# Performance work log

Measured on AMD Instinct MI355X. Metric: run time of the kernel, lower is better.

The kernel has to match this reference:

```python
import math
import jax, jax.numpy as jnp
import numpy as np

B, N, W, D, H = 16, 64, 128, 128, 4

def posenc(L, d):
    pos = jnp.arange(L, dtype=jnp.float32)[:, None]
    div = jnp.exp(jnp.arange(0, d, 2, dtype=jnp.float32) * (-math.log(10000.0) / d))
    pe = jnp.zeros((L, d), jnp.float32)
    pe = pe.at[:, 0::2].set(jnp.sin(pos * div))
    pe = pe.at[:, 1::2].set(jnp.cos(pos * div))
    return pe

def ln(x):
    # torch nn.LayerNorm(x.shape[1:]) created fresh each call: normalize over all non-batch dims, no affine
    ax = tuple(range(1, x.ndim))
    m = x.mean(ax, keepdims=True)
    v = ((x - m) ** 2).mean(ax, keepdims=True)
    return (x - m) / jnp.sqrt(v + 1e-5)

def conv1d(x, w, b):
    # x [B,C,L], w [Cout,Cin,K] (torch layout), VALID padding
    y = jax.lax.conv_general_dilated(x, w, (1,), 'VALID', dimension_numbers=('NCH', 'OIH', 'NCH'))
    return y + b[None, :, None]

def convt1d(x, w, b, stride, pad):
    # torch ConvTranspose1d, w [Cin,Cout,K]
    K = w.shape[2]
    w_ = jnp.flip(w, 2).transpose(1, 0, 2)  # [Cout,Cin,K]
    y = jax.lax.conv_general_dilated(x, w_, (1,), [(K - 1 - pad, K - 1 - pad)],
                                     lhs_dilation=(stride,), dimension_numbers=('NCH', 'OIH', 'NCH'))
    return y + b[None, :, None]

def mha(q, k, v, wi, bi, wo, bo):
    # torch nn.MultiheadAttention(batch_first=True), H heads
    d = q.shape[-1]
    qp = q @ wi[:d].T + bi[:d]
    kp = k @ wi[d:2 * d].T + bi[d:2 * d]
    vp = v @ wi[2 * d:].T + bi[2 * d:]
    def heads(t):
        b_, l_, _ = t.shape
        return t.reshape(b_, l_, H, d // H).transpose(0, 2, 1, 3)
    qh, kh, vh = heads(qp), heads(kp), heads(vp)
    s = jnp.einsum('bhqd,bhkd->bhqk', qh, kh) / jnp.sqrt(jnp.asarray(d // H, qh.dtype))
    o = jnp.einsum('bhqk,bhkd->bhqd', jax.nn.softmax(s, -1), vh)
    b_, l_ = q.shape[0], q.shape[1]
    return o.transpose(0, 2, 1, 3).reshape(b_, l_, d) @ wo.T + bo


def setup_inputs():
    key = jax.random.key(0)
    ks = iter(jax.random.split(key, 64))
    def w(shape, s=0.05):
        return jax.random.normal(next(ks), shape, jnp.float32) * s
    inp = {}
    inp['tokens'] = jax.random.randint(next(ks), (B, N, W), 0, 257, jnp.int32)
    inp['emb_table'] = w((257, D), 1.0)
    for nm in ['ce', 'ct', 'cg', 'ces', 'cts']:
        inp['w_' + nm] = w((D, D, 3))
        inp['b_' + nm] = w((D,))
    inp['mha_wi'] = w((3 * D, D)); inp['mha_bi'] = w((3 * D,))
    inp['mha_wo'] = w((D, D)); inp['mha_bo'] = w((D,))
    s = 1.0 / math.sqrt(D)
    inp['tgt1'] = jax.random.uniform(next(ks), (1, D), jnp.float32, -s, s)
    inp['tgt2'] = jax.random.uniform(next(ks), (1, D), jnp.float32, -s, s)
    for nm in ['mu', 'lv', 'di']:
        inp['w_' + nm] = w((D, D)); inp['b_' + nm] = w((D,))
    inp['eps'] = jax.random.normal(next(ks), (B, D), jnp.float32)
    inp['dk_w'] = w((32, 32)); inp['dk_b'] = w((32,))
    inp['dv_w'] = w((32, 32)); inp['dv_b'] = w((32,))
    inp['wt1'] = w((32, 64, 3)); inp['bt1'] = w((64,))
    inp['wt2'] = w((64, 128, 3)); inp['bt2'] = w((128,))
    for nm in ['sq', 'sk', 'sv']:
        inp[nm + '_w'] = w((128, 128)); inp[nm + '_b'] = w((128,))
    inp['wt3'] = w((128, 128, 3)); inp['bt3'] = w((128,))
    return inp


def reference(tokens, emb_table, w_ce, b_ce, w_ct, b_ct, w_cg, b_cg, w_ces, b_ces, w_cts, b_cts,
              mha_wi, mha_bi, mha_wo, mha_bo, tgt1, tgt2,
              w_mu, b_mu, w_lv, b_lv, w_di, b_di, eps,
              dk_w, dk_b, dv_w, dv_b, wt1, bt1, wt2, bt2,
              sq_w, sq_b, sk_w, sk_b, sv_w, sv_b, wt3, bt3):
    emb = emb_table[tokens] + posenc(W, D)                    # [B,N,W,D]
    flat = emb.reshape(B * N, W, D)                           # batch the per-sample torch loop

    def word_branch(wc, bc, act):
        h = act(conv1d(flat.transpose(0, 2, 1), wc, bc)).transpose(0, 2, 1)  # [BN,W-2,D]
        return mha(h, h, h, mha_wi, mha_bi, mha_wo, mha_bo)

    a_e = jax.nn.elu(word_branch(w_ce, b_ce, jax.nn.elu))
    a_t = jnp.tanh(word_branch(w_ct, b_ct, jnp.tanh))
    xw = ln((a_e * a_t).reshape(B, N, W - 2, D)).reshape(B * N, W - 2, D)

    h = jax.nn.elu(conv1d(xw.transpose(0, 2, 1), w_cg, b_cg)).transpose(0, 2, 1)  # [BN,W-4,D]
    q1 = jnp.broadcast_to(tgt1[None], (B * N, 1, D))
    out = mha(q1, h, h, mha_wi, mha_bi, mha_wo, mha_bo)[:, 0, :].reshape(B, N, D)

    se = out + posenc(N, D)                                   # sentence level

    def sent_branch(wc, bc, act):
        hh = act(conv1d(se.transpose(0, 2, 1), wc, bc)).transpose(0, 2, 1)       # [B,N-2,D]
        return mha(hh, hh, hh, mha_wi, mha_bi, mha_wo, mha_bo)

    s_e = jax.nn.elu(sent_branch(w_ces, b_ces, jax.nn.elu))
    s_t = jnp.tanh(sent_branch(w_cts, b_cts, jnp.tanh))
    xs = ln(s_e * s_t)
    q2 = jnp.broadcast_to(tgt2[None], (B, 1, D))
    doc = mha(q2, xs, xs, mha_wi, mha_bi, mha_wo, mha_bo)[:, 0, :]

    mu = doc @ w_mu.T + b_mu
    lv = doc @ w_lv.T + b_lv
    z = mu + eps * jnp.exp(0.5 * lv)

    h = (z @ w_di.T + b_di).reshape(B, 32, -1)                # [B,32,4]
    L = h.shape[2]
    k = jnp.einsum('oi,bil->bol', dk_w, h) + dk_b[None, :, None]
    v = jnp.einsum('oi,bil->bol', dv_w, h) + dv_b[None, :, None]
    kh = k.reshape(B, H, 8, L)
    vh = v.reshape(B, H, 8, L)
    att = jax.nn.softmax(jnp.einsum('bhdl,bhdm->bhlm', kh, vh) / jnp.sqrt(8.0), -1)
    h = jax.nn.elu(jnp.einsum('bhlm,bhdm->bhld', att, vh).reshape(B, 32, L))
    h = jax.nn.elu(ln(convt1d(h, wt1, bt1, 2, 1)))            # [B,64,7]
    h = jax.nn.elu(ln(convt1d(h, wt2, bt2, 2, 1)))            # [B,128,13]
    L2 = h.shape[2]
    qc = jnp.einsum('oi,bil->bol', sq_w, h) + sq_b[None, :, None]
    kc = jnp.einsum('oi,bil->bol', sk_w, h) + sk_b[None, :, None]
    vc = jnp.einsum('oi,bil->bol', sv_w, h) + sv_b[None, :, None]
    qh = qc.reshape(B, H, 32, L2)
    khh = kc.reshape(B, H, 32, L2)
    att = jax.nn.softmax(jnp.einsum('bhdl,bhdm->bhlm', qh, khh) / jnp.sqrt(32.0), -1)
    vr = vc.reshape(B, H, 32, L2).reshape(B, H, L2, 32)       # faithful torch .view reinterpretation
    h = jax.nn.elu(jnp.einsum('bhlm,bhmd->bhld', att, vr).reshape(B, 128, L2))
    recon = jax.nn.sigmoid(ln(convt1d(h, wt3, bt3, 1, 1)))    # [B,128,13]
    return recon, mu, lv
```

## Files before the change

### kernel.cpp

```cpp
#include <hip/hip_runtime.h>
#include <hip/hip_bf16.h>

typedef __hip_bfloat16 bf16;
typedef __attribute__((ext_vector_type(8))) short bf16x8;
typedef __attribute__((ext_vector_type(4))) float f32x4;

__device__ __forceinline__ float b2f(bf16 x){ return __bfloat162float(x); }
__device__ __forceinline__ bf16  f2b(float x){ return __float2bfloat16(x); }
__device__ __forceinline__ unsigned short b2u(bf16 x){ union{bf16 b; unsigned short u;} c; c.b = x; return c.u; }

#define LOG2E 1.4426950408889634f
#define QSC (0.17677669529663687f * LOG2E)

#define GLD16(gp, lp) __builtin_amdgcn_global_load_lds( \
    (const __attribute__((address_space(1))) void*)(gp), \
    (__attribute__((address_space(3))) void*)(lp), 16, 0, 0)

__device__ __forceinline__ float fexp2(float x){
  float r; asm("v_exp_f32 %0, %1" : "=v"(r) : "v"(x)); return r;
}
__device__ __forceinline__ float fast_exp(float x){ return fexp2(x * LOG2E); }
__device__ __forceinline__ float eluf(float x){ return x > 0.f ? x : fast_exp(x) - 1.f; }
__device__ __forceinline__ float fast_tanh(float x){
  float cx = fminf(fmaxf(x, -15.f), 15.f);
  float t = fexp2(cx * (2.f*LOG2E));
  return (t - 1.f) / (t + 1.f);
}

#define PE_C (-0.07195578415606394f)

__device__ __forceinline__ float pe_val(int pos, int d){
  int j2 = d & ~1;
  float ang = (float)pos * expf((float)j2 * PE_C);
  return (d & 1) ? cosf(ang) : sinf(ang);
}

__device__ __forceinline__ void pack_one(const float* __restrict__ W, bf16* __restrict__ out,
                                         int K, int N, int conv, int qscale, int t){
  int j = t & 7, lane = (t >> 3) & 63;
  int rest = t >> 9; int NT = N >> 4;
  int nt = rest % NT; int kb = rest / NT;
  int k = kb*32 + ((lane >> 4) << 3) + j;
  int n = nt*16 + (lane & 15);
  float v = conv ? W[n*384 + (k & 127)*3 + (k >> 7)] : W[(long)n*K + k];
  if (qscale && n < 128) v *= QSC;
  out[t] = f2b(v);
}

__global__ void k_prep(const float* __restrict__ w_ce, const float* __restrict__ w_ct,
                       const float* __restrict__ w_cg, const float* __restrict__ w_ces,
                       const float* __restrict__ w_cts, const float* __restrict__ wi,
                       const float* __restrict__ wo,
                       bf16* P_CE, bf16* P_CT, bf16* P_CG, bf16* P_CES, bf16* P_CTS,
                       bf16* P_WI, bf16* P_WO, float* __restrict__ pet){
  int bid = blockIdx.x;
  if (bid < 1152){
    int grp = bid / 192; int t = (bid % 192)*256 + threadIdx.x;
    const float* W; bf16* out; int K, N, conv, qs = 0;
    if      (grp == 0){ W = w_ce;  out = P_CE;  K=384; N=128; conv=1; }
    else if (grp == 1){ W = w_ct;  out = P_CT;  K=384; N=128; conv=1; }
    else if (grp == 2){ W = w_cg;  out = P_CG;  K=384; N=128; conv=1; }
    else if (grp == 3){ W = w_ces; out = P_CES; K=384; N=128; conv=1; }
    else if (grp == 4){ W = w_cts; out = P_CTS; K=384; N=128; conv=1; }
    else              { W = wi;    out = P_WI;  K=128; N=384; conv=0; qs=1; }
    pack_one(W, out, K, N, conv, qs, t);
  } else if (bid < 1216){
    int t = (bid - 1152)*256 + threadIdx.x;
    pack_one(wo, P_WO, 128, 128, 0, 0, t);
  } else {
    int i = (bid - 1216)*256 + threadIdx.x;
    if (i < 16384) pet[i] = pe_val(i >> 7, i & 127);
  }
}

__global__ void k_qprep(const float* __restrict__ wi, const float* __restrict__ bi,
                        const float* __restrict__ t1, const float* __restrict__ t2,
                        float* __restrict__ rkv){
  int tid = threadIdx.x;
  __shared__ float qps[256];
  {
    int which = tid >> 7, jj = tid & 127;
    const float* t = which ? t2 : t1;
    float a = bi[jj];
    for (int i = 0; i < 128; ++i) a += wi[jj*128 + i] * t[i];
    qps[tid] = a;
  }
  __syncthreads();
  int i = tid & 127, which = tid >> 7;
  for (int h = 0; h < 4; ++h){
    float a = 0.f;
    for (int d = 0; d < 32; ++d) a += qps[which*128 + h*32 + d] * wi[(128 + h*32 + d)*128 + i];
    rkv[which*512 + h*128 + i] = a;
  }
}

__global__ void k_embed8(const int* __restrict__ tok, const float* __restrict__ tab,
                         const float* __restrict__ pet, bf16* __restrict__ out){
  int t = blockIdx.x*256 + threadIdx.x;
  int q = t & 15;
  int flat = t >> 4; int w = flat & 127;
  int tk = tok[flat];
  const float* ta = tab + tk*128 + q*8;
  const float* pe = pet + (w << 7) + q*8;
  bf16 ob[8];
  #pragma unroll
  for (int i = 0; i < 8; ++i) ob[i] = f2b(ta[i] + pe[i]);
  *(f32x4*)(out + (size_t)t*8) = *(f32x4*)ob;
}

__global__ void k_se(const bf16* __restrict__ in, const float* __restrict__ pet, bf16* __restrict__ out){
  int idx = blockIdx.x*256 + threadIdx.x;
  int d = idx & 127; int n = (idx >> 7) & 63;
  out[idx] = f2b(b2f(in[idx]) + pet[(n << 7) + d]);
}

template<bool GLL>
__global__ __launch_bounds__(256)
void k_gemm_mfma(const bf16* __restrict__ A, const bf16* __restrict__ Bp_, const bf16* __restrict__ Bp2,
                 const float* __restrict__ bias_, const float* __restrict__ bias2,
                 bf16* __restrict__ C_, bf16* __restrict__ C2p,
                 const bf16* __restrict__ mul,
                 int M, int K, int a_lout, int a_lind, int lda,
                 int NT, int n0t, int ldc, int act_, int act2,
                 const float* __restrict__ lnst, int lngrp){
  const bf16* Bp = Bp_; const float* bias = bias_; bf16* C = C_; int act = act_;
  if (blockIdx.z){ Bp = Bp2; bias = bias2; C = C2p; act = act2; }

  __shared__ f32x4 AsV[2][512];
  char* As0 = (char*)AsV[0];
  char* As1 = (char*)AsV[1];
  int tid = threadIdx.x;
  int lane = tid & 63, wave = tid >> 6;
  int wm = wave >> 1, wn = wave & 1;
  int m0 = blockIdx.x*128;
  int by = blockIdx.y;

  long offA[2]; bool okA[2]; float lnm[2], lnr[2]; int sbyte[2];
  #pragma unroll
  for (int p = 0; p < 2; ++p){
    int e = tid + p*256;
    int row, kq;
    if (GLL){
      int x = e;
      row = (((x >> 3) << 1) | (((x >> 2) ^ (x >> 4)) & 1)) & 127;
      kq  = ((((x >> 1) ^ (x >> 3)) & 1) << 1) | ((x ^ (x >> 2) ^ (x >> 4)) & 1);
    } else {
      row = e >> 2; kq = e & 3;
    }
    int m = m0 + row;
    okA[p] = (m < M);
    long off = 0;
    if (okA[p]){
      off = (a_lout > 0) ? (long)(m / a_lout)*a_lind + (long)(m % a_lout)*128 + kq*8
                         : (long)m*lda + kq*8;
    }
    offA[p] = off;
    lnm[p] = 0.f; lnr[p] = 1.f;
    if (!GLL && lnst && okA[p]){ int g = (int)(off / (long)lngrp); lnm[p] = lnst[2*g]; lnr[p] = lnst[2*g+1]; }
    sbyte[p] = (row*64 + kq*16) ^ ((row & 7) << 4);
  }

  const bf16* bptr[4];
  size_t bstep = (size_t)NT*512;
  #pragma unroll
  for (int fn = 0; fn < 4; ++fn){
    int ntile = n0t + by*8 + wn*4 + fn;
    bptr[fn] = Bp + ((size_t)ntile*64 + lane)*8;
  }
  int abyte[4];
  #pragma unroll
  for (int fm = 0; fm < 4; ++fm){
    int row = wm*64 + fm*16 + (lane & 15);
    abyte[fm] = (row*64 + ((lane >> 4) << 4)) ^ ((row & 7) << 4);
  }

  f32x4 acc[4][4];
  #pragma unroll
  for (int i = 0; i < 4; ++i)
    #pragma unroll
    for (int j = 0; j < 4; ++j) acc[i][j] = (f32x4){0.f,0.f,0.f,0.f};

  int nk = K >> 5;

  if constexpr (GLL){
    int ldsw = (tid >> 6)*1024;
    #pragma unroll
    for (int p = 0; p < 2; ++p)
      GLD16(A + offA[p], As0 + p*4096 + ldsw);
    __syncthreads();
    for (int kb = 0; kb < nk; ++kb){
      char* cur = (kb & 1) ? As1 : As0;
      char* nxt = (kb & 1) ? As0 : As1;
      bool more = (kb + 1) < nk;
      if (more){
        #pragma unroll
        for (int p = 0; p < 2; ++p)
          GLD16(A + offA[p] + (kb+1)*32, nxt + p*4096 + ldsw);
      }
      bf16x8 bfr[4];
      #pragma unroll
      for (int fn = 0; fn < 4; ++fn) bfr[fn] = *(const bf16x8*)(bptr[fn] + (size_t)kb*bstep);
      bf16x8 afr[4];
      #pragma unroll
      for (int fm = 0; fm < 4; ++fm) afr[fm] = *(const bf16x8*)(cur + abyte[fm]);
      #pragma unroll
      for (int fm = 0; fm < 4; ++fm)
        #pragma unroll
        for (int fn = 0; fn < 4; ++fn)
          acc[fm][fn] = __builtin_amdgcn_mfma_f32_16x16x32_bf16(afr[fm], bfr[fn], acc[fm][fn], 0, 0, 0);
      __syncthreads();
    }
  } else {
    auto loadA = [&](int p, int kb)->float4{
      float4 v = make_float4(0.f,0.f,0.f,0.f);
      if (okA[p]){
        v = *(const float4*)(A + offA[p] + kb*32);
        if (lnst){
          bf16* pp = (bf16*)&v; bf16 oo[8];
          #pragma unroll
          for (int u = 0; u < 8; ++u) oo[u] = f2b((b2f(pp[u]) - lnm[p]) * lnr[p]);
          v = *(float4*)&oo[0];
        }
      }
      return v;
    };
    float4 va0 = loadA(0, 0), va1 = loadA(1, 0);
    *(float4*)(As0 + sbyte[0]) = va0;
    *(float4*)(As0 + sbyte[1]) = va1;
    __syncthreads();
    for (int kb = 0; kb < nk; ++kb){
      char* cur = (kb & 1) ? As1 : As0;
      char* nxt = (kb & 1) ? As0 : As1;
      bool more = (kb + 1) < nk;
      if (more){ va0 = loadA(0, kb+1); va1 = loadA(1, kb+1); }
      bf16x8 bfr[4];
      #pragma unroll
      for (int fn = 0; fn < 4; ++fn) bfr[fn] = *(const bf16x8*)(bptr[fn] + (size_t)kb*bstep);
      bf16x8 afr[4];
      #pragma unroll
      for (int fm = 0; fm < 4; ++fm) afr[fm] = *(const bf16x8*)(cur + abyte[fm]);
      #pragma unroll
      for (int fm = 0; fm < 4; ++fm)
        #pragma unroll
        for (int fn = 0; fn < 4; ++fn)
          acc[fm][fn] = __builtin_amdgcn_mfma_f32_16x16x32_bf16(afr[fm], bfr[fn], acc[fm][fn], 0, 0, 0);
      if (more){
        *(float4*)(nxt + sbyte[0]) = va0;
        *(float4*)(nxt + sbyte[1]) = va1;
      }
      __syncthreads();
    }
  }

  #pragma unroll
  for (int fm = 0; fm < 4; ++fm){
    #pragma unroll
    for (int r = 0; r < 4; ++r){
      int m = m0 + wm*64 + fm*16 + ((lane >> 4) << 2) + r;
      if (m >= M) continue;
      #pragma unroll
      for (int fn = 0; fn < 4; ++fn){
        int n = by*128 + wn*64 + fn*16 + (lane & 15);
        float v = acc[fm][fn][r] + (bias ? bias[n] : 0.f);
        if (act == 1) v = eluf(v);
        else if (act == 2) v = fast_tanh(v);
        if (mul) v *= b2f(mul[(long)m*ldc + n]);
        C[(long)m*ldc + n] = f2b(v);
      }
    }
  }
}

template<int L>
__global__ __launch_bounds__(256)
void k_attn_fused(const bf16* __restrict__ X, const bf16* __restrict__ Pwi,
                  const float* __restrict__ bi, bf16* __restrict__ o){
  constexpr int KB  = (L + 31) / 32;
  constexpr int MT  = KB * 2;
  constexpr int WMT = MT / 4;
  constexpr int NP  = KB * 32;
  constexpr int PRS = NP * 2;

  __shared__ alignas(16) char As[NP*256];
  __shared__ alignas(16) char Qb[NP*64];
  __shared__ alignas(16) char Kb[NP*64];
  __shared__ alignas(16) char Vt[32*PRS];
  char* Pb = As;

  int tid = threadIdx.x;
  int s = blockIdx.x >> 2, h = blockIdx.x & 3;
  const bf16* xb = X + (size_t)s*L*128;

  {
    constexpr int NCH = (NP*16)/256;
    int ldsw = (tid >> 6)*1024;
    #pragma unroll
    for (int p = 0; p < NCH; ++p){
      int x = p*256 + tid;
      int row = x >> 4;
      int c = (x & 15) ^ (row & 7);
      const bf16* gp = (row < L) ? (xb + (size_t)row*128 + c*8) : xb;
      GLD16(gp, As + p*4096 + ldsw);
    }
  }
  __syncthreads();

  int lane = tid & 63, wave = tid >> 6;
  int col = lane & 15;

  __builtin_amdgcn_s_setprio(1);
  #pragma unroll
  for (int mt = 0; mt < WMT; ++mt){
    int mtile = wave*WMT + mt;
    int arow = mtile*16 + col;
    bf16x8 a4[4];
    #pragma unroll
    for (int kb = 0; kb < 4; ++kb)
      a4[kb] = *(const bf16x8*)(As + ((arow*256 + kb*64 + ((lane >> 4) << 4)) ^ ((arow & 7) << 4)));
    #pragma unroll
    for (int which = 0; which < 3; ++which){
      f32x4 av[2];
      #pragma unroll
      for (int nt = 0; nt < 2; ++nt){
        int ntile = which*8 + h*2 + nt;
        float bia = bi[which*128 + h*32 + nt*16 + col];
        if (which == 0) bia *= QSC;
        av[nt] = (f32x4){bia, bia, bia, bia};
        #pragma unroll
        for (int kb = 0; kb < 4; ++kb){
          bf16x8 bfr = *(const bf16x8*)(Pwi + (((size_t)kb*24 + ntile)*64 + lane)*8);
          av[nt] = __builtin_amdgcn_mfma_f32_16x16x32_bf16(a4[kb], bfr, av[nt], 0, 0, 0);
        }
      }
      #pragma unroll
      for (int r = 0; r < 4; ++r){
        int row = mtile*16 + ((lane >> 4) << 2) + r;
        if (which < 2){
          unsigned pk = (unsigned)b2u(f2b(av[0][r])) | ((unsigned)b2u(f2b(av[1][r])) << 16);
          char* dst = which ? Kb : Qb;
          *(unsigned*)(dst + ((row*64 + col*4) ^ ((row & 7) << 4))) = pk;
        } else {
          int pos = (row & 15)*MT + (row >> 4);
          #pragma unroll
          for (int nt = 0; nt < 2; ++nt){
            int d = nt*16 + col;
            *(bf16*)(Vt + ((d*PRS + pos*2) ^ ((d & 7) << 4))) = f2b(av[nt][r]);
          }
        }
      }
    }
  }
  __builtin_amdgcn_s_setprio(0);
  __syncthreads();

  f32x4 acc[WMT][MT];
  #pragma unroll
  for (int mt = 0; mt < WMT; ++mt)
    #pragma unroll
    for (int nt = 0; nt < MT; ++nt) acc[mt][nt] = (f32x4){0.f,0.f,0.f,0.f};

  bf16x8 af[WMT];
  #pragma unroll
  for (int mt = 0; mt < WMT; ++mt){
    int row = (wave*WMT + mt)*16 + col;
    af[mt] = *(const bf16x8*)(Qb + ((row*64 + ((lane >> 4) << 4)) ^ ((row & 7) << 4)));
  }
  __builtin_amdgcn_s_setprio(1);
  #pragma unroll
  for (int nt = 0; nt < MT; ++nt){
    int rk2 = nt*16 + col;
    bf16x8 bfk = *(const bf16x8*)(Kb + ((rk2*64 + ((lane >> 4) << 4)) ^ ((rk2 & 7) << 4)));
    #pragma unroll
    for (int mt = 0; mt < WMT; ++mt)
      acc[mt][nt] = __builtin_amdgcn_mfma_f32_16x16x32_bf16(af[mt], bfk, acc[mt][nt], 0, 0, 0);
  }
  __builtin_amdgcn_s_setprio(0);

  const bool lastMask = col >= (L - (MT-1)*16);
  float pinv[WMT][4];
  #pragma unroll
  for (int mt = 0; mt < WMT; ++mt){
    #pragma unroll
    for (int r = 0; r < 4; ++r){
      float mx = -1e30f;
      #pragma unroll
      for (int nt = 0; nt < MT; ++nt){
        float v = acc[mt][nt][r];
        if (nt == MT-1 && lastMask){ v = -1e30f; acc[mt][nt][r] = v; }
        mx = fmaxf(mx, v);
      }
      mx = fmaxf(mx, __shfl_xor(mx, 1));
      mx = fmaxf(mx, __shfl_xor(mx, 2));
      mx = fmaxf(mx, __shfl_xor(mx, 4));
      mx = fmaxf(mx, __shfl_xor(mx, 8));
      float sum = 0.f;
      bf16 prow[MT];
      #pragma unroll
      for (int nt = 0; nt < MT; ++nt){
        float p = fexp2(acc[mt][nt][r] - mx);
        prow[nt] = f2b(p);
        sum += p;
      }
      sum += __shfl_xor(sum, 1);
      sum += __shfl_xor(sum, 2);
      sum += __shfl_xor(sum, 4);
      sum += __shfl_xor(sum, 8);
      pinv[mt][r] = 1.f / sum;
      int row = (wave*WMT + mt)*16 + ((lane >> 4) << 2) + r;
      char* dst = Pb + ((row*PRS + col*(MT*2)) ^ ((row & 7) << 4));
      if constexpr (MT == 8) *(f32x4*)dst = *(f32x4*)prow;
      else                   *(float2*)dst = *(float2*)prow;
    }
  }

  #pragma unroll
  for (int mt = 0; mt < WMT; ++mt){
    int mtile = wave*WMT + mt;
    f32x4 o0 = (f32x4){0.f,0.f,0.f,0.f}, o1 = (f32x4){0.f,0.f,0.f,0.f};
    __builtin_amdgcn_s_setprio(1);
    #pragma unroll
    for (int kb = 0; kb < KB; ++kb){
      int row = mtile*16 + col;
      bf16x8 pa = *(const bf16x8*)(Pb + ((row*PRS + kb*64 + ((lane >> 4) << 4)) ^ ((row & 7) << 4)));
      int d0 = col;
      bf16x8 v0 = *(const bf16x8*)(Vt + ((d0*PRS + kb*64 + ((lane >> 4) << 4)) ^ ((d0 & 7) << 4)));
      bf16x8 v1 = *(const bf16x8*)(Vt + (((d0+16)*PRS + kb*64 + ((lane >> 4) << 4)) ^ (((d0+16) & 7) << 4)));
      o0 = __builtin_amdgcn_mfma_f32_16x16x32_bf16(pa, v0, o0, 0, 0, 0);
      o1 = __builtin_amdgcn_mfma_f32_16x16x32_bf16(pa, v1, o1, 0, 0, 0);
    }
    __builtin_amdgcn_s_setprio(0);
    #pragma unroll
    for (int r = 0; r < 4; ++r){
      int row = mtile*16 + ((lane >> 4) << 2) + r;
      if (row < L){
        size_t ob = ((size_t)s*L + row)*128 + h*32 + col;
        o[ob]      = f2b(o0[r] * pinv[mt][r]);
        o[ob + 16] = f2b(o1[r] * pinv[mt][r]);
      }
    }
  }
}

template<int L>
__global__ __launch_bounds__(256)
void k_attn_tgt(const bf16* __restrict__ hin, const float* __restrict__ rk,
                const float* __restrict__ wi, const float* __restrict__ bi,
                bf16* __restrict__ outp){
  __shared__ alignas(16) char Hs[L*256];
  __shared__ float RKs[512];
  __shared__ float Ps[512];
  __shared__ float Cs[512];
  int tid = threadIdx.x, lane = tid & 63, wave = tid >> 6;
  int s = blockIdx.x;
  const bf16* hb = hin + (size_t)s*L*128;
  for (int e = tid; e < L*16; e += 256){
    int row = e >> 4, c = e & 15;
    *(float4*)(Hs + row*256 + ((c ^ (row & 7)) << 4)) = *(const float4*)(hb + row*128 + c*8);
  }
  for (int e = tid; e < 512; e += 256) RKs[e] = rk[e];
  __syncthreads();

  int j0 = lane, j1 = lane + 64;
  float v0 = -1e30f, v1 = -1e30f;
  if (j0 < L){
    float a = 0.f;
    #pragma unroll
    for (int c = 0; c < 16; ++c){
      bf16x8 x = *(const bf16x8*)(Hs + j0*256 + ((c ^ (j0 & 7)) << 4));
      #pragma unroll
      for (int u = 0; u < 8; ++u) a += b2f(((bf16*)&x)[u]) * RKs[wave*128 + c*8 + u];
    }
    v0 = a * 0.17677669529663687f;
  }
  if (j1 < L){
    float a = 0.f;
    #pragma unroll
    for (int c = 0; c < 16; ++c){
      bf16x8 x = *(const bf16x8*)(Hs + j1*256 + ((c ^ (j1 & 7)) << 4));
      #pragma unroll
      for (int u = 0; u < 8; ++u) a += b2f(((bf16*)&x)[u]) * RKs[wave*128 + c*8 + u];
    }
    v1 = a * 0.17677669529663687f;
  }
  float mx = fmaxf(v0, v1);
  #pragma unroll
  for (int off = 32; off; off >>= 1) mx = fmaxf(mx, __shfl_xor(mx, off));
  float e0 = (j0 < L) ? fast_exp(v0 - mx) : 0.f;
  float e1 = (j1 < L) ? fast_exp(v1 - mx) : 0.f;
  float sum = e0 + e1;
  #pragma unroll
  for (int off = 32; off; off >>= 1) sum += __shfl_xor(sum, off);
  float inv = 1.f / sum;
  Ps[wave*128 + j0] = e0 * inv;
  Ps[wave*128 + j1] = e1 * inv;

  int i0 = lane*2;
  float c0 = 0.f, c1 = 0.f;
  for (int j = 0; j < L; ++j){
    float p = Ps[wave*128 + j];
    short2 w2 = *(const short2*)(Hs + j*256 + (((i0 >> 3) ^ (j & 7)) << 4) + (i0 & 7)*2);
    c0 += p * b2f(*(bf16*)&w2.x);
    c1 += p * b2f(*(bf16*)&w2.y);
  }
  Cs[wave*128 + i0]     = c0;
  Cs[wave*128 + i0 + 1] = c1;
  __syncthreads();

  if (tid < 128){
    int h2 = tid >> 5;
    float a = bi[256 + tid];
    const float* wr = wi + (size_t)(256 + tid)*128;
    for (int i = 0; i < 128; ++i) a += wr[i] * Cs[h2*128 + i];
    outp[(size_t)s*128 + tid] = f2b(a);
  }
}

__global__ void k_ln_partial(const bf16* __restrict__ x, float* __restrict__ part, int GS, int P){
  int pi = blockIdx.x % P;
  int chunk8 = GS / P / 8;
  size_t base = (size_t)(blockIdx.x / P)*GS + (size_t)pi*(GS/P);
  float s = 0.f, s2 = 0.f;
  for (int i = threadIdx.x; i < chunk8; i += 256){
    f32x4 raw = *(const f32x4*)(x + base + (size_t)i*8);
    const bf16* xb = (const bf16*)&raw;
    #pragma unroll
    for (int j = 0; j < 8; ++j){ float v = b2f(xb[j]); s += v; s2 += v*v; }
  }
  #pragma unroll
  for (int off = 32; off; off >>= 1){ s += __shfl_xor(s, off); s2 += __shfl_xor(s2, off); }
  __shared__ float sh[8];
  int lane = threadIdx.x & 63, wv = threadIdx.x >> 6;
  if (lane == 0){ sh[wv] = s; sh[4 + wv] = s2; }
  __syncthreads();
  if (threadIdx.x == 0){
    part[blockIdx.x*2]     = sh[0]+sh[1]+sh[2]+sh[3];
    part[blockIdx.x*2 + 1] = sh[4]+sh[5]+sh[6]+sh[7];
  }
}

__global__ void k_ln_fin(const float* __restrict__ part, float* __restrict__ stats, int P, int GS){
  int g = blockIdx.x;
  float s = 0.f, s2 = 0.f;
  for (int i = threadIdx.x; i < P; i += 256){ s += part[(g*P + i)*2]; s2 += part[(g*P + i)*2 + 1]; }
  #pragma unroll
  for (int off = 32; off; off >>= 1){ s += __shfl_xor(s, off); s2 += __shfl_xor(s2, off); }
  __shared__ float sh[8];
  int lane = threadIdx.x & 63, wv = threadIdx.x >> 6;
  if (lane == 0){ sh[wv] = s; sh[4 + wv] = s2; }
  __syncthreads();
  if (threadIdx.x == 0){
    float S = sh[0]+sh[1]+sh[2]+sh[3], S2 = sh[4]+sh[5]+sh[6]+sh[7];
    float mean = S / GS;
    float var = S2 / GS - mean*mean;
    stats[g*2] = mean; stats[g*2 + 1] = rsqrtf(var + 1e-5f);
  }
}

__global__ void k_ln_small_bf16(const bf16* __restrict__ x, bf16* __restrict__ y, int n){
  int g = blockIdx.x;
  const bf16* xb = x + (size_t)g*n;
  bf16* yb = y + (size_t)g*n;
  float s = 0.f, s2 = 0.f;
  for (int i = threadIdx.x; i < n; i += 256){ float v = b2f(xb[i]); s += v; s2 += v*v; }
  #pragma unroll
  for (int off = 32; off; off >>= 1){ s += __shfl_xor(s, off); s2 += __shfl_xor(s2, off); }
  __shared__ float sh[8];  __shared__ float ms[2];
  int lane = threadIdx.x & 63, wv = threadIdx.x >> 6;
  if (lane == 0){ sh[wv] = s; sh[4 + wv] = s2; }
  __syncthreads();
  if (threadIdx.x == 0){
    float S = sh[0]+sh[1]+sh[2]+sh[3], S2 = sh[4]+sh[5]+sh[6]+sh[7];
    float mean = S / n;
    ms[0] = mean; ms[1] = rsqrtf(S2 / n - mean*mean + 1e-5f);
  }
  __syncthreads();
  float mean = ms[0], inv = ms[1];
  for (int i = threadIdx.x; i < n; i += 256) yb[i] = f2b((b2f(xb[i]) - mean)*inv);
}

__global__ void k_ln_small_f32(const float* __restrict__ x, float* __restrict__ y, int n, int act){
  int g = blockIdx.x;
  const float* xb = x + (size_t)g*n;
  float* yb = y + (size_t)g*n;
  float s = 0.f, s2 = 0.f;
  for (int i = threadIdx.x; i < n; i += 256){ float v = xb[i]; s += v; s2 += v*v; }
  #pragma unroll
  for (int off = 32; off; off >>= 1){ s += __shfl_xor(s, off); s2 += __shfl_xor(s2, off); }
  __shared__ float sh[8];  __shared__ float ms[2];
  int lane = threadIdx.x & 63, wv = threadIdx.x >> 6;
  if (lane == 0){ sh[wv] = s; sh[4 + wv] = s2; }
  __syncthreads();
  if (threadIdx.x == 0){
    float S = sh[0]+sh[1]+sh[2]+sh[3], S2 = sh[4]+sh[5]+sh[6]+sh[7];
    float mean = S / n;
    ms[0] = mean; ms[1] = rsqrtf(S2 / n - mean*mean + 1e-5f);
  }
  __syncthreads();
  float mean = ms[0], inv = ms[1];
  for (int i = threadIdx.x; i < n; i += 256){
    float v = (xb[i] - mean)*inv;
    if (act == 1) v = eluf(v);
    else if (act == 3) v = 1.f/(1.f + fast_exp(-v));
    yb[i] = v;
  }
}

__global__ __launch_bounds__(256)
void k_dec_a(const bf16* __restrict__ DOC,
             const float* __restrict__ w_mu, const float* __restrict__ b_mu,
             const float* __restrict__ w_lv, const float* __restrict__ b_lv,
             const float* __restrict__ eps,
             const float* __restrict__ w_di, const float* __restrict__ b_di,
             const float* __restrict__ dk_w, const float* __restrict__ dk_b,
             const float* __restrict__ dv_w, const float* __restrict__ dv_b,
             const float* __restrict__ wt1, const float* __restrict__ bt1,
             float* __restrict__ dout, float* __restrict__ DEC2){
  int b = blockIdx.x, tid = threadIdx.x;
  __shared__ float Zs[128], H3[128], KD[128], VD[128], D1[128];
  __shared__ float C1[448];
  __shared__ float sc[64];
  __shared__ float red[8], ms[2];

  if (tid < 128){
    const bf16* dr = DOC + b*128;
    float mu = b_mu[tid], lv = b_lv[tid];
    for (int i = 0; i < 128; ++i){
      float x = b2f(dr[i]);
      mu += x * w_mu[tid*128 + i];
      lv += x * w_lv[tid*128 + i];
    }
    dout[26624 + b*128 + tid] = mu;
    dout[28672 + b*128 + tid] = lv;
    Zs[tid] = mu + eps[b*128 + tid] * fast_exp(0.5f*lv);
  }
  __syncthreads();
  if (tid < 128){
    float a = b_di[tid];
    for (int i = 0; i < 128; ++i) a += Zs[i] * w_di[tid*128 + i];
    H3[tid] = a;
  }
  __syncthreads();
  if (tid < 128){
    int l = tid & 3, o2 = tid >> 2;
    float ak = dk_b[o2], av = dv_b[o2];
    for (int i = 0; i < 32; ++i){
      float xv = H3[i*4 + l];
      ak += dk_w[o2*32 + i]*xv;
      av += dv_w[o2*32 + i]*xv;
    }
    KD[tid] = ak; VD[tid] = av;
  }
  __syncthreads();
  if (tid < 64){
    int h = tid >> 4, l = (tid >> 2) & 3, m = tid & 3;
    float a = 0.f;
    #pragma unroll
    for (int d = 0; d < 8; ++d) a += KD[(h*8+d)*4 + l] * VD[(h*8+d)*4 + m];
    sc[tid] = a * 0.35355339059327373f;
  }
  __syncthreads();
  if (tid < 16){
    int base = tid*4;
    float mx = fmaxf(fmaxf(sc[base],sc[base+1]),fmaxf(sc[base+2],sc[base+3]));
    float e0=fast_exp(sc[base]-mx), e1=fast_exp(sc[base+1]-mx), e2=fast_exp(sc[base+2]-mx), e3=fast_exp(sc[base+3]-mx);
    float inv = 1.f/(e0+e1+e2+e3);
    sc[base]=e0*inv; sc[base+1]=e1*inv; sc[base+2]=e2*inv; sc[base+3]=e3*inv;
  }
  __syncthreads();
  if (tid < 128){
    int h = tid >> 5, rem = tid & 31, l = rem >> 3, d = rem & 7;
    float a = 0.f;
    #pragma unroll
    for (int m = 0; m < 4; ++m) a += sc[h*16 + l*4 + m] * VD[(h*8+d)*4 + m];
    D1[tid] = eluf(a);
  }
  __syncthreads();
  for (int idx = tid; idx < 448; idx += 256){
    int co = idx / 7, lo = idx % 7;
    float a = bt1[co];
    for (int k = 0; k < 3; ++k){
      int t = lo + 1 - k;
      if (t < 0 || (t & 1)) continue;
      int li = t >> 1; if (li >= 4) continue;
      float aa = 0.f;
      for (int ci = 0; ci < 32; ++ci) aa += D1[ci*4 + li] * wt1[ci*192 + co*3 + k];
      a += aa;
    }
    C1[idx] = a;
  }
  __syncthreads();
  {
    float s = 0.f, s2 = 0.f;
    for (int i = tid; i < 448; i += 256){ float v = C1[i]; s += v; s2 += v*v; }
    #pragma unroll
    for (int o = 32; o; o >>= 1){ s += __shfl_xor(s, o); s2 += __shfl_xor(s2, o); }
    int lane = tid & 63, wv = tid >> 6;
    if (lane == 0){ red[wv] = s; red[4+wv] = s2; }
    __syncthreads();
    if (tid == 0){
      float S = red[0]+red[1]+red[2]+red[3], S2 = red[4]+red[5]+red[6]+red[7];
      float mean = S/448.f; ms[0] = mean; ms[1] = rsqrtf(S2/448.f - mean*mean + 1e-5f);
    }
    __syncthreads();
    float mean = ms[0], inv = ms[1];
    for (int i = tid; i < 448; i += 256)
      DEC2[b*448 + i] = eluf((C1[i]-mean)*inv);
  }
}

__global__ void k_chanproj3(const float* __restrict__ x,
                            const float* __restrict__ w1, const float* __restrict__ b1,
                            const float* __restrict__ w2, const float* __restrict__ b2,
                            const float* __restrict__ w3, const float* __restrict__ b3,
                            float* __restrict__ y1, float* __restrict__ y2, float* __restrict__ y3,
                            int Bn, int C, int L){
  int idx = blockIdx.x*256 + threadIdx.x;
  if (idx >= Bn*C*L) return;
  int l = idx % L; int t2 = idx / L; int o = t2 % C; int b = t2 / C;
  float a1 = b1[o], a2 = b2[o], a3 = b3[o];
  const float* xb = x + (size_t)b*C*L + l;
  for (int i = 0; i < C; ++i){
    float xv = xb[i*L];
    a1 += w1[(size_t)o*C + i]*xv;
    a2 += w2[(size_t)o*C + i]*xv;
    a3 += w3[(size_t)o*C + i]*xv;
  }
  y1[idx] = a1; y2[idx] = a2; y3[idx] = a3;
}

__global__ __launch_bounds__(256)
void k_dec_attn2(const float* __restrict__ qc, const float* __restrict__ kc,
                 const float* __restrict__ vc, float* __restrict__ out){
  int b = blockIdx.x >> 2, h = blockIdx.x & 3, tid = threadIdx.x;
  __shared__ float sc[169];
  const float* qb = qc + b*1664 + h*416;
  const float* kb = kc + b*1664 + h*416;
  const float* vb = vc + b*1664 + h*416;
  if (tid < 169){
    int l = tid/13, m = tid - l*13;
    float a = 0.f;
    #pragma unroll
    for (int d = 0; d < 32; ++d) a += qb[d*13 + l] * kb[d*13 + m];
    sc[tid] = a * 0.17677669529663687f;
  }
  __syncthreads();
  if (tid < 13){
    float mx = -1e30f;
    for (int m = 0; m < 13; ++m) mx = fmaxf(mx, sc[tid*13 + m]);
    float s = 0.f;
    for (int m = 0; m < 13; ++m){ float p = fast_exp(sc[tid*13 + m] - mx); sc[tid*13 + m] = p; s += p; }
    float inv = 1.f/s;
    for (int m = 0; m < 13; ++m) sc[tid*13 + m] *= inv;
  }
  __syncthreads();
  for (int idx = tid; idx < 416; idx += 256){
    int l = idx >> 5, d = idx & 31;
    float a = 0.f;
    for (int m = 0; m < 13; ++m) a += sc[l*13 + m] * vb[m*32 + d];
    out[b*1664 + h*416 + idx] = eluf(a);
  }
}

__global__ __launch_bounds__(256)
void k_convt(const float* __restrict__ x, const float* __restrict__ w,
             const float* __restrict__ bias, float* __restrict__ y,
             int Bn, int Ci, int Co, int Lin, int Lout, int stride, int pad, int nch){
  __shared__ float xs[1664];
  int b = blockIdx.x / nch;
  int c0 = (blockIdx.x % nch)*16;
  int tid = threadIdx.x;
  for (int i = tid; i < Ci*Lin; i += 256) xs[i] = x[(size_t)b*Ci*Lin + i];
  __syncthreads();
  int co = c0 + (tid & 15);
  int lo = tid >> 4;
  if (co >= Co || lo >= Lout) return;
  float a = bias[co];
  for (int k = 0; k < 3; ++k){
    int t = lo + pad - k;
    if (t < 0 || (t % stride)) continue;
    int li = t / stride;
    if (li >= Lin) continue;
    float aa = 0.f;
    for (int ci = 0; ci < Ci; ++ci) aa += xs[ci*Lin + li] * w[(size_t)ci*Co*3 + co*3 + k];
    a += aa;
  }
  y[(size_t)b*Co*Lout + co*Lout + lo] = a;
}

extern "C" void kernel_launch(void* const* d_in, const int* in_sizes, int n_in,
                              void* d_out, int out_size, void* d_ws, size_t ws_size,
                              hipStream_t stream){
  const int*   tokens = (const int*)  d_in[0];
  const float* tab    = (const float*)d_in[1];
  const float* w_ce = (const float*)d_in[2];  const float* b_ce = (const float*)d_in[3];
  const float* w_ct = (const float*)d_in[4];  const float* b_ct = (const float*)d_in[5];
  const float* w_cg = (const float*)d_in[6];  const float* b_cg = (const float*)d_in[7];
  const float* w_ces= (const float*)d_in[8];  const float* b_ces= (const float*)d_in[9];
  const float* w_cts= (const float*)d_in[10]; const float* b_cts= (const float*)d_in[11];
  const float* wi   = (const float*)d_in[12]; const float* bi   = (const float*)d_in[13];
  const float* wo   = (const float*)d_in[14]; const float* bo   = (const float*)d_in[15];
  const float* tgt1 = (const float*)d_in[16]; const float* tgt2 = (const float*)d_in[17];
  const float* w_mu = (const float*)d_in[18]; const float* b_mu = (const float*)d_in[19];
  const float* w_lv = (const float*)d_in[20]; const float* b_lv = (const float*)d_in[21];
  const float* w_di = (const float*)d_in[22]; const float* b_di = (const float*)d_in[23];
  const float* epsb = (const float*)d_in[24];
  const float* dk_w = (const float*)d_in[25]; const float* dk_b = (const float*)d_in[26];
  const float* dv_w = (const float*)d_in[27]; const float* dv_b = (const float*)d_in[28];
  const float* wt1  = (const float*)d_in[29]; const float* bt1  = (const float*)d_in[30];
  const float* wt2  = (const float*)d_in[31]; const float* bt2  = (const float*)d_in[32];
  const float* sq_w = (const float*)d_in[33]; const float* sq_b = (const float*)d_in[34];
  const float* sk_w = (const float*)d_in[35]; const float* sk_b = (const float*)d_in[36];
  const float* sv_w = (const float*)d_in[37]; const float* sv_b = (const float*)d_in[38];
  const float* wt3  = (const float*)d_in[39]; const float* bt3  = (const float*)d_in[40];

  float* dout = (float*)d_out;

  char* ws = (char*)d_ws;
  size_t off = 0;
  auto take = [&](size_t bytes)->char*{ char* p = ws + off; off += (bytes + 255) & ~(size_t)255; return p; };
  bf16* EMB  = (bf16*)take(16777216ull*2);
  bf16* HB   = (bf16*)take(16515072ull*2);
  bf16* OB   = (bf16*)take(16515072ull*2);
  bf16* AE   = (bf16*)take(16515072ull*2);
  bf16* O1   = (bf16*)take(131072ull*2);
  bf16* OUTB = (bf16*)take(131072ull*2);
  bf16* SEB  = (bf16*)take(131072ull*2);
  bf16* SH   = (bf16*)take(126976ull*2);
  bf16* SCT  = (bf16*)take(126976ull*2);
  bf16* SO   = (bf16*)take(126976ull*2);
  bf16* SAE  = (bf16*)take(126976ull*2);
  bf16* XS   = (bf16*)take(126976ull*2);
  bf16* DO1  = (bf16*)take(2048ull*2);
  bf16* DOC  = (bf16*)take(2048ull*2);
  float* RK  = (float*)take(1024*4);
  float* PART= (float*)take(2016ull*2*4);
  float* STATS=(float*)take(32*4);
  float* DEC2= (float*)take(7168*4);
  float* C2  = (float*)take(26624*4);
  float* DEC3= (float*)take(26624*4);
  float* QC  = (float*)take(26624*4);
  float* KC  = (float*)take(26624*4);
  float* VC  = (float*)take(26624*4);
  float* DEC4= (float*)take(26624*4);
  float* C3  = (float*)take(26624*4);
  float* PET = (float*)take(16384*4);
  bf16* P_CE = (bf16*)take(49152ull*2);
  bf16* P_CT = (bf16*)take(49152ull*2);
  bf16* P_CG = (bf16*)take(49152ull*2);
  bf16* P_CES= (bf16*)take(49152ull*2);
  bf16* P_CTS= (bf16*)take(49152ull*2);
  bf16* P_WI = (bf16*)take(49152ull*2);
  bf16* P_WO = (bf16*)take(16384ull*2);
  (void)ws_size; (void)in_sizes; (void)n_in; (void)out_size;

  auto cdiv = [](long a, long b){ return (int)((a + b - 1)/b); };
  auto gemm = [&](const bf16* A, const bf16* Bpp, const float* bias, bf16* C, const bf16* mul,
                  int M, int N, int K, int a_lout, int a_lind, int lda, int NT, int n0t, int ldc, int act,
                  const float* lnst, int lngrp){
    dim3 g(cdiv(M,128), N/128, 1);
    if (lnst)
      k_gemm_mfma<false><<<g, 256, 0, stream>>>(A, Bpp, Bpp, bias, bias, C, C, mul,
                                                M, K, a_lout, a_lind, lda, NT, n0t, ldc, act, act, lnst, lngrp);
    else
      k_gemm_mfma<true><<<g, 256, 0, stream>>>(A, Bpp, Bpp, bias, bias, C, C, mul,
                                               M, K, a_lout, a_lind, lda, NT, n0t, ldc, act, act, nullptr, 0);
  };
  auto gemmz = [&](const bf16* A, const bf16* Bp1, const float* b1, bf16* C1, int act1,
                   const bf16* Bp2, const float* b2, bf16* C2p, int act2,
                   int M, int N, int K, int a_lout, int a_lind, int lda, int NT, int n0t, int ldc){
    dim3 g(cdiv(M,128), N/128, 2);
    k_gemm_mfma<true><<<g, 256, 0, stream>>>(A, Bp1, Bp2, b1, b2, C1, C2p, nullptr,
                                             M, K, a_lout, a_lind, lda, NT, n0t, ldc, act1, act2, nullptr, 0);
  };

  k_prep<<<1280, 256, 0, stream>>>(w_ce, w_ct, w_cg, w_ces, w_cts, wi, wo,
                                   P_CE, P_CT, P_CG, P_CES, P_CTS, P_WI, P_WO, PET);
  k_qprep<<<1, 256, 0, stream>>>(wi, bi, tgt1, tgt2, RK);
  k_embed8<<<8192, 256, 0, stream>>>(tokens, tab, PET, EMB);

  gemmz(EMB, P_CE, b_ce, HB, 1, P_CT, b_ct, OB, 2, 129024, 128, 384, 126, 16384, 0, 8, 0, 128);

  k_attn_fused<126><<<4096, 256, 0, stream>>>(HB, P_WI, bi, EMB);
  gemm(EMB, P_WO, bo, AE, nullptr, 129024, 128, 128, 0, 0, 128, 8, 0, 128, 1, nullptr, 0);

  k_attn_fused<126><<<4096, 256, 0, stream>>>(OB, P_WI, bi, EMB);
  gemm(EMB, P_WO, bo, HB, AE, 129024, 128, 128, 0, 0, 128, 8, 0, 128, 2, nullptr, 0);

  k_ln_partial<<<2016, 256, 0, stream>>>(HB, PART, 1032192, 126);
  k_ln_fin<<<16, 256, 0, stream>>>(PART, STATS, 126, 1032192);

  gemm(HB, P_CG, b_cg, OB, nullptr, 126976, 128, 384, 124, 16128, 0, 8, 0, 128, 1, STATS, 1032192);

  k_attn_tgt<124><<<1024, 256, 0, stream>>>(OB, RK, wi, bi, O1);
  gemm(O1, P_WO, bo, OUTB, nullptr, 1024, 128, 128, 0, 0, 128, 8, 0, 128, 0, nullptr, 0);

  k_se<<<512, 256, 0, stream>>>(OUTB, PET, SEB);

  gemmz(SEB, P_CES, b_ces, SH, 1, P_CTS, b_cts, SCT, 2, 992, 128, 384, 62, 8192, 0, 8, 0, 128);

  k_attn_fused<62><<<64, 256, 0, stream>>>(SH, P_WI, bi, SO);
  gemm(SO, P_WO, bo, SAE, nullptr, 992, 128, 128, 0, 0, 128, 8, 0, 128, 1, nullptr, 0);

  k_attn_fused<62><<<64, 256, 0, stream>>>(SCT, P_WI, bi, SO);
  gemm(SO, P_WO, bo, SH, SAE, 992, 128, 128, 0, 0, 128, 8, 0, 128, 2, nullptr, 0);

  k_ln_small_bf16<<<16, 256, 0, stream>>>(SH, XS, 7936);

  k_attn_tgt<62><<<16, 256, 0, stream>>>(XS, RK + 512, wi, bi, DO1);
  gemm(DO1, P_WO, bo, DOC, nullptr, 16, 128, 128, 0, 0, 128, 8, 0, 128, 0, nullptr, 0);

  k_dec_a<<<16, 256, 0, stream>>>(DOC, w_mu, b_mu, w_lv, b_lv, epsb, w_di, b_di,
                                  dk_w, dk_b, dv_w, dv_b, wt1, bt1, dout, DEC2);
  k_convt<<<16*8, 256, 0, stream>>>(DEC2, wt2, bt2, C2, 16, 64, 128, 7, 13, 2, 1, 8);
  k_ln_small_f32<<<16, 256, 0, stream>>>(C2, DEC3, 1664, 1);
  k_chanproj3<<<cdiv(26624,256), 256, 0, stream>>>(DEC3, sq_w, sq_b, sk_w, sk_b, sv_w, sv_b,
                                                   QC, KC, VC, 16, 128, 13);
  k_dec_attn2<<<64, 256, 0, stream>>>(QC, KC, VC, DEC4);
  k_convt<<<16*8, 256, 0, stream>>>(DEC4, wt3, bt3, C3, 16, 128, 128, 13, 13, 1, 1, 8);
  k_ln_small_f32<<<16, 256, 0, stream>>>(C3, dout, 1664, 3);
}
```

Baseline: 629.5 us.

## Fuse embedding gather, positional add, and LayerNorm partial sums into GEMM kernels

Removes the standalone embedding kernel: the first conv GEMM now gathers token embeddings and adds positional encodings inside its A-tile load, using the non-LDS-direct path. Removes the separate positional-add kernel by adding the positional term in the output-projection GEMM epilogue. Removes the LayerNorm partial-sum pass by accumulating per-block sums and sums of squares in the preceding GEMM epilogue, with 63 partials per group instead of 126. This saves large intermediate writes and reads, but the first GEMM loses its global-to-LDS direct loads and does scattered fp32 table reads.

```diff
diff --git a/kernel.cpp b/kernel.cpp
--- a/kernel.cpp
+++ b/kernel.cpp
@@ -94,26 +94,6 @@
   }
 }
 
-__global__ void k_embed8(const int* __restrict__ tok, const float* __restrict__ tab,
-                         const float* __restrict__ pet, bf16* __restrict__ out){
-  int t = blockIdx.x*256 + threadIdx.x;
-  int q = t & 15;
-  int flat = t >> 4; int w = flat & 127;
-  int tk = tok[flat];
-  const float* ta = tab + tk*128 + q*8;
-  const float* pe = pet + (w << 7) + q*8;
-  bf16 ob[8];
-  #pragma unroll
-  for (int i = 0; i < 8; ++i) ob[i] = f2b(ta[i] + pe[i]);
-  *(f32x4*)(out + (size_t)t*8) = *(f32x4*)ob;
-}
-
-__global__ void k_se(const bf16* __restrict__ in, const float* __restrict__ pet, bf16* __restrict__ out){
-  int idx = blockIdx.x*256 + threadIdx.x;
-  int d = idx & 127; int n = (idx >> 7) & 63;
-  out[idx] = f2b(b2f(in[idx]) + pet[(n << 7) + d]);
-}
-
 template<bool GLL>
 __global__ __launch_bounds__(256)
 void k_gemm_mfma(const bf16* __restrict__ A, const bf16* __restrict__ Bp_, const bf16* __restrict__ Bp2,
@@ -122,11 +102,15 @@
                  const bf16* __restrict__ mul,
                  int M, int K, int a_lout, int a_lind, int lda,
                  int NT, int n0t, int ldc, int act_, int act2,
-                 const float* __restrict__ lnst, int lngrp){
+                 const float* __restrict__ lnst, int lngrp,
+                 const int* __restrict__ tok, const float* __restrict__ tabp,
+                 const float* __restrict__ petp, const float* __restrict__ sepe,
+                 float* __restrict__ part){
   const bf16* Bp = Bp_; const float* bias = bias_; bf16* C = C_; int act = act_;
   if (blockIdx.z){ Bp = Bp2; bias = bias2; C = C2p; act = act2; }
 
   __shared__ f32x4 AsV[2][512];
+  __shared__ float redp[16];
   char* As0 = (char*)AsV[0];
   char* As1 = (char*)AsV[1];
   int tid = threadIdx.x;
@@ -214,12 +198,25 @@
     auto loadA = [&](int p, int kb)->float4{
       float4 v = make_float4(0.f,0.f,0.f,0.f);
       if (okA[p]){
-        v = *(const float4*)(A + offA[p] + kb*32);
-        if (lnst){
-          bf16* pp = (bf16*)&v; bf16 oo[8];
+        long e = offA[p] + kb*32;
+        if (tok){
+          int seq = (int)(e >> 14); int rest = (int)e & 16383;
+          int wrow = rest >> 7, d0 = rest & 127;
+          int t = tok[(seq << 7) + wrow];
+          const float* ta = tabp + t*128 + d0;
+          const float* pe = petp + (wrow << 7) + d0;
+          bf16 oo[8];
           #pragma unroll
-          for (int u = 0; u < 8; ++u) oo[u] = f2b((b2f(pp[u]) - lnm[p]) * lnr[p]);
+          for (int u = 0; u < 8; ++u) oo[u] = f2b(ta[u] + pe[u]);
           v = *(float4*)&oo[0];
+        } else {
+          v = *(const float4*)(A + e);
+          if (lnst){
+            bf16* pp = (bf16*)&v; bf16 oo[8];
+            #pragma unroll
+            for (int u = 0; u < 8; ++u) oo[u] = f2b((b2f(pp[u]) - lnm[p]) * lnr[p]);
+            v = *(float4*)&oo[0];
+          }
         }
       }
       return v;
@@ -252,6 +249,7 @@
     }
   }
 
+  float ps = 0.f, ps2 = 0.f;
   #pragma unroll
   for (int fm = 0; fm < 4; ++fm){
     #pragma unroll
@@ -265,8 +263,20 @@
         if (act == 1) v = eluf(v);
         else if (act == 2) v = fast_tanh(v);
         if (mul) v *= b2f(mul[(long)m*ldc + n]);
+        if (sepe) v += sepe[(m & 63)*128 + n];
+        if (part){ ps += v; ps2 += v*v; }
         C[(long)m*ldc + n] = f2b(v);
       }
+    }
+  }
+  if (part){
+    #pragma unroll
+    for (int o = 32; o; o >>= 1){ ps += __shfl_xor(ps, o); ps2 += __shfl_xor(ps2, o); }
+    if (lane == 0){ redp[wave] = ps; redp[8 + wave] = ps2; }
+    __syncthreads();
+    if (tid == 0){
+      part[blockIdx.x*2]     = redp[0]+redp[1]+redp[2]+redp[3];
+      part[blockIdx.x*2 + 1] = redp[8]+redp[9]+redp[10]+redp[11];
     }
   }
 }
@@ -512,29 +522,6 @@
     const float* wr = wi + (size_t)(256 + tid)*128;
     for (int i = 0; i < 128; ++i) a += wr[i] * Cs[h2*128 + i];
     outp[(size_t)s*128 + tid] = f2b(a);
-  }
-}
-
-__global__ void k_ln_partial(const bf16* __restrict__ x, float* __restrict__ part, int GS, int P){
-  int pi = blockIdx.x % P;
-  int chunk8 = GS / P / 8;
-  size_t base = (size_t)(blockIdx.x / P)*GS + (size_t)pi*(GS/P);
-  float s = 0.f, s2 = 0.f;
-  for (int i = threadIdx.x; i < chunk8; i += 256){
-    f32x4 raw = *(const f32x4*)(x + base + (size_t)i*8);
-    const bf16* xb = (const bf16*)&raw;
-    #pragma unroll
-    for (int j = 0; j < 8; ++j){ float v = b2f(xb[j]); s += v; s2 += v*v; }
-  }
-  #pragma unroll
-  for (int off = 32; off; off >>= 1){ s += __shfl_xor(s, off); s2 += __shfl_xor(s2, off); }
-  __shared__ float sh[8];
-  int lane = threadIdx.x & 63, wv = threadIdx.x >> 6;
-  if (lane == 0){ sh[wv] = s; sh[4 + wv] = s2; }
-  __syncthreads();
-  if (threadIdx.x == 0){
-    part[blockIdx.x*2]     = sh[0]+sh[1]+sh[2]+sh[3];
-    part[blockIdx.x*2 + 1] = sh[4]+sh[5]+sh[6]+sh[7];
   }
 }
 
@@ -823,7 +810,6 @@
   bf16* OB   = (bf16*)take(16515072ull*2);
   bf16* AE   = (bf16*)take(16515072ull*2);
   bf16* O1   = (bf16*)take(131072ull*2);
-  bf16* OUTB = (bf16*)take(131072ull*2);
   bf16* SEB  = (bf16*)take(131072ull*2);
   bf16* SH   = (bf16*)take(126976ull*2);
   bf16* SCT  = (bf16*)take(126976ull*2);
@@ -833,7 +819,7 @@
   bf16* DO1  = (bf16*)take(2048ull*2);
   bf16* DOC  = (bf16*)take(2048ull*2);
   float* RK  = (float*)take(1024*4);
-  float* PART= (float*)take(2016ull*2*4);
+  float* PART= (float*)take(1008ull*2*4);
   float* STATS=(float*)take(32*4);
   float* DEC2= (float*)take(7168*4);
   float* C2  = (float*)take(26624*4);
@@ -856,58 +842,65 @@
   auto cdiv = [](long a, long b){ return (int)((a + b - 1)/b); };
   auto gemm = [&](const bf16* A, const bf16* Bpp, const float* bias, bf16* C, const bf16* mul,
                   int M, int N, int K, int a_lout, int a_lind, int lda, int NT, int n0t, int ldc, int act,
-                  const float* lnst, int lngrp){
+                  const float* lnst, int lngrp, const float* sepe, float* part){
     dim3 g(cdiv(M,128), N/128, 1);
     if (lnst)
       k_gemm_mfma<false><<<g, 256, 0, stream>>>(A, Bpp, Bpp, bias, bias, C, C, mul,
-                                                M, K, a_lout, a_lind, lda, NT, n0t, ldc, act, act, lnst, lngrp);
+                                                M, K, a_lout, a_lind, lda, NT, n0t, ldc, act, act, lnst, lngrp,
+                                                nullptr, nullptr, nullptr, sepe, part);
     else
       k_gemm_mfma<true><<<g, 256, 0, stream>>>(A, Bpp, Bpp, bias, bias, C, C, mul,
-                                               M, K, a_lout, a_lind, lda, NT, n0t, ldc, act, act, nullptr, 0);
+                                               M, K, a_lout, a_lind, lda, NT, n0t, ldc, act, act, nullptr, 0,
+                                               nullptr, nullptr, nullptr, sepe, part);
+  };
+  auto gemmz_emb = [&](const bf16* Bp1, const float* b1, bf16* C1, int act1,
+                       const bf16* Bp2, const float* b2, bf16* C2p, int act2,
+                       int M, int N, int K, int a_lout, int a_lind, int NT, int ldc){
+    dim3 g(cdiv(M,128), N/128, 2);
+    k_gemm_mfma<false><<<g, 256, 0, stream>>>(nullptr, Bp1, Bp2, b1, b2, C1, C2p, nullptr,
+                                              M, K, a_lout, a_lind, 0, NT, 0, ldc, act1, act2, nullptr, 0,
+                                              tokens, tab, PET, nullptr, nullptr);
   };
   auto gemmz = [&](const bf16* A, const bf16* Bp1, const float* b1, bf16* C1, int act1,
                    const bf16* Bp2, const float* b2, bf16* C2p, int act2,
                    int M, int N, int K, int a_lout, int a_lind, int lda, int NT, int n0t, int ldc){
     dim3 g(cdiv(M,128), N/128, 2);
     k_gemm_mfma<true><<<g, 256, 0, stream>>>(A, Bp1, Bp2, b1, b2, C1, C2p, nullptr,
-                                             M, K, a_lout, a_lind, lda, NT, n0t, ldc, act1, act2, nullptr, 0);
+                                             M, K, a_lout, a_lind, lda, NT, n0t, ldc, act1, act2, nullptr, 0,
+                                             nullptr, nullptr, nullptr, nullptr, nullptr);
   };
 
   k_prep<<<1280, 256, 0, stream>>>(w_ce, w_ct, w_cg, w_ces, w_cts, wi, wo,
                                    P_CE, P_CT, P_CG, P_CES, P_CTS, P_WI, P_WO, PET);
   k_qprep<<<1, 256, 0, stream>>>(wi, bi, tgt1, tgt2, RK);
-  k_embed8<<<8192, 256, 0, stream>>>(tokens, tab, PET, EMB);
-
-  gemmz(EMB, P_CE, b_ce, HB, 1, P_CT, b_ct, OB, 2, 129024, 128, 384, 126, 16384, 0, 8, 0, 128);
+
+  gemmz_emb(P_CE, b_ce, HB, 1, P_CT, b_ct, OB, 2, 129024, 128, 384, 126, 16384, 8, 128);
 
   k_attn_fused<126><<<4096, 256, 0, stream>>>(HB, P_WI, bi, EMB);
-  gemm(EMB, P_WO, bo, AE, nullptr, 129024, 128, 128, 0, 0, 128, 8, 0, 128, 1, nullptr, 0);
+  gemm(EMB, P_WO, bo, AE, nullptr, 129024, 128, 128, 0, 0, 128, 8, 0, 128, 1, nullptr, 0, nullptr, nullptr);
 
   k_attn_fused<126><<<4096, 256, 0, stream>>>(OB, P_WI, bi, EMB);
-  gemm(EMB, P_WO, bo, HB, AE, 129024, 128, 128, 0, 0, 128, 8, 0, 128, 2, nullptr, 0);
-
-  k_ln_partial<<<2016, 256, 0, stream>>>(HB, PART, 1032192, 126);
-  k_ln_fin<<<16, 256, 0, stream>>>(PART, STATS, 126, 1032192);
-
-  gemm(HB, P_CG, b_cg, OB, nullptr, 126976, 128, 384, 124, 16128, 0, 8, 0, 128, 1, STATS, 1032192);
+  gemm(EMB, P_WO, bo, HB, AE, 129024, 128, 128, 0, 0, 128, 8, 0, 128, 2, nullptr, 0, nullptr, PART);
+
+  k_ln_fin<<<16, 256, 0, stream>>>(PART, STATS, 63, 1032192);
+
+  gemm(HB, P_CG, b_cg, OB, nullptr, 126976, 128, 384, 124, 16128, 0, 8, 0, 128, 1, STATS, 1032192, nullptr, nullptr);
 
   k_attn_tgt<124><<<1024, 256, 0, stream>>>(OB, RK, wi, bi, O1);
-  gemm(O1, P_WO, bo, OUTB, nullptr, 1024, 128, 128, 0, 0, 128, 8, 0, 128, 0, nullptr, 0);
-
-  k_se<<<512, 256, 0, stream>>>(OUTB, PET, SEB);
+  gemm(O1, P_WO, bo, SEB, nullptr, 1024, 128, 128, 0, 0, 128, 8, 0, 128, 0, nullptr, 0, PET, nullptr);
 
   gemmz(SEB, P_CES, b_ces, SH, 1, P_CTS, b_cts, SCT, 2, 992, 128, 384, 62, 8192, 0, 8, 0, 128);
 
   k_attn_fused<62><<<64, 256, 0, stream>>>(SH, P_WI, bi, SO);
-  gemm(SO, P_WO, bo, SAE, nullptr, 992, 128, 128, 0, 0, 128, 8, 0, 128, 1, nullptr, 0);
+  gemm(SO, P_WO, bo, SAE, nullptr, 992, 128, 128, 0, 0, 128, 8, 0, 128, 1, nullptr, 0, nullptr, nullptr);
 
   k_attn_fused<62><<<64, 256, 0, stream>>>(SCT, P_WI, bi, SO);
-  gemm(SO, P_WO, bo, SH, SAE, 992, 128, 128, 0, 0, 128, 8, 0, 128, 2, nullptr, 0);
+  gemm(SO, P_WO, bo, SH, SAE, 992, 128, 128, 0, 0, 128, 8, 0, 128, 2, nullptr, 0, nullptr, nullptr);
 
   k_ln_small_bf16<<<16, 256, 0, stream>>>(SH, XS, 7936);
 
   k_attn_tgt<62><<<16, 256, 0, stream>>>(XS, RK + 512, wi, bi, DO1);
-  gemm(DO1, P_WO, bo, DOC, nullptr, 16, 128, 128, 0, 0, 128, 8, 0, 128, 0, nullptr, 0);
+  gemm(DO1, P_WO, bo, DOC, nullptr, 16, 128, 128, 0, 0, 128, 8, 0, 128, 0, nullptr, 0, nullptr, nullptr);
 
   k_dec_a<<<16, 256, 0, stream>>>(DOC, w_mu, b_mu, w_lv, b_lv, epsb, w_di, b_di,
                                   dk_w, dk_b, dv_w, dv_b, wt1, bt1, dout, DEC2);
```

New measurement: 668.7 us. +6.2%, slower.
